# Optimization experiments

Hardware: AMD Instinct MI355X
Metric: run time of the kernel (lower is better)

## Reference

```python
import jax, jax.numpy as jnp
import numpy as np


def setup_inputs() -> dict:
    key = jax.random.key(0)
    ks = jax.random.split(key, 8)
    B, N, D = 8, 2048, 128
    s = 1.0 / float(np.sqrt(D))
    node = jax.random.normal(ks[0], (B, N, D), dtype=jnp.float32)
    node_mask = jax.random.randint(ks[1], (B, N), 0, 2, dtype=jnp.int32)
    punctuation_graph = jax.random.randint(ks[2], (B, N, N), 0, 2, dtype=jnp.int32)
    w_nw = jax.random.uniform(ks[3], (1, D), jnp.float32, -s, s)
    b_nw = jax.random.uniform(ks[4], (1,), jnp.float32, -s, s)
    w_self = jax.random.uniform(ks[5], (D, D), jnp.float32, -s, s)
    b_self = jax.random.uniform(ks[6], (D,), jnp.float32, -s, s)
    w_punct = jax.random.uniform(ks[7], (D, D), jnp.float32, -s, s)
    return {"node": node, "node_mask": node_mask, "punctuation_graph": punctuation_graph,
            "w_nw": w_nw, "b_nw": b_nw, "w_self": w_self, "b_self": b_self,
            "w_punct": w_punct, "iteration_steps": 2}


def reference(node, node_mask, punctuation_graph, w_nw, b_nw, w_self, b_self, w_punct, iteration_steps):
    B, N, D = node.shape
    # dd_graph = mask outer product with zeroed diagonal; graph = dd_graph * punctuation_graph
    eye = jnp.eye(N, dtype=punctuation_graph.dtype)
    dd = node_mask[:, None, :] * node_mask[:, :, None] * (1 - eye)[None, :, :]  # [B,N,N]
    graph = dd * punctuation_graph  # [B,N,N] int, binary
    nbr_num = graph.sum(-1)  # [B,N]
    # replace_masked_values(nbr_num, nbr_num>=1, 1): nodes with no neighbors get denom 1
    nbr_f = jnp.where(nbr_num >= 1, nbr_num.astype(node.dtype), jnp.asarray(1.0, node.dtype))
    gmask = graph > 0
    weights = []
    x = node
    for _ in range(iteration_steps):  # small fixed step count
        dw = jax.nn.sigmoid(jnp.einsum('bnd,od->bno', x, w_nw) + b_nw)[..., 0]  # [B,N]
        weights.append(dw)
        self_info = jnp.einsum('bnd,ed->bne', x, w_self) + b_self  # [B,N,D]
        info_p = jnp.einsum('bnd,ed->bne', x, w_punct)  # [B,N,D]
        # node_weight[b,i,j] = dw[b,j] where graph[b,i,j] else 0
        nw = jnp.where(gmask, dw[:, None, :], jnp.asarray(0.0, x.dtype))  # [B,N,N]
        agg = jnp.einsum('bnm,bmd->bnd', nw, info_p) / nbr_f[..., None]
        x = jax.nn.relu(self_info + agg)
    all_weight = jnp.stack(weights, axis=1)  # [B, steps, N]
    return x, all_weight
```

## Files before the change

kernel.cpp:

```cpp
#include <hip/hip_runtime.h>
#include <hip/hip_bf16.h>

#define BB 8
#define NN 2048
#define DD 128

typedef __attribute__((ext_vector_type(8))) __bf16 bf16x8;
typedef __attribute__((ext_vector_type(4))) float f32x4;
typedef __attribute__((ext_vector_type(4))) int   i32x4;

static __device__ __forceinline__ unsigned short f2bf(float f) {
    union { float f; unsigned u; } v; v.f = f;
    unsigned r = (v.u + 0x7FFFu + ((v.u >> 16) & 1u)) >> 16;
    return (unsigned short)r;
}
static __device__ __forceinline__ float bf2f(unsigned short b) {
    union { unsigned u; float f; } v; v.u = ((unsigned)b) << 16;
    return v.f;
}

__global__ __launch_bounds__(256) void kernB0(
    const float* __restrict__ x,
    const float* __restrict__ w_nw, const float* __restrict__ b_nw,
    const float* __restrict__ w_self, const float* __restrict__ b_self,
    const float* __restrict__ w_punct,
    float* __restrict__ si_out,
    unsigned short* __restrict__ yne_out,
    unsigned short* __restrict__ yT_out,
    float* __restrict__ aw_out)
{
    __shared__ unsigned short xt[64*32];
    __shared__ unsigned short wst[128*32];
    __shared__ unsigned short wpt[128*32];
    __shared__ float wnw_l[DD];
    __shared__ float red[256];
    __shared__ float dw_l[64];
    __shared__ unsigned short ytl[128*72];

    const int n0 = blockIdx.x * 64;
    const int t  = threadIdx.x;
    const int b  = n0 >> 11;
    const int nb = n0 & (NN - 1);

    if (t < DD) wnw_l[t] = w_nw[t];
    __syncthreads();

    const int wave = t >> 6, lane = t & 63;
    const int wm = wave >> 1, wn = wave & 1;
    const int quad = lane >> 4, l16 = lane & 15;

    const int n_loc = t >> 2, dq = t & 3;
    const int we = t >> 1,   wh = t & 1;

    f32x4 accs[2][4] = {}; f32x4 accp[2][4] = {};
    float dwpart = 0.f;

    #pragma unroll
    for (int kk = 0; kk < 4; ++kk) {
        const int k0 = kk * 32;
        {
            const float* xs = x + (size_t)(n0 + n_loc) * DD + k0 + dq * 8;
            f32x4 a = *(const f32x4*)xs;
            f32x4 c = *(const f32x4*)(xs + 4);
            const float* wv = &wnw_l[k0 + dq * 8];
            dwpart += a.x*wv[0] + a.y*wv[1] + a.z*wv[2] + a.w*wv[3]
                    + c.x*wv[4] + c.y*wv[5] + c.z*wv[6] + c.w*wv[7];
            unsigned q0 = f2bf(a.x) | ((unsigned)f2bf(a.y) << 16);
            unsigned q1 = f2bf(a.z) | ((unsigned)f2bf(a.w) << 16);
            unsigned q2 = f2bf(c.x) | ((unsigned)f2bf(c.y) << 16);
            unsigned q3 = f2bf(c.z) | ((unsigned)f2bf(c.w) << 16);
            i32x4 pw = {(int)q0,(int)q1,(int)q2,(int)q3};
            *(i32x4*)&xt[n_loc*32 + dq*8] = pw;
        }
        {
            const float* s1 = w_self  + (size_t)we * DD + k0 + wh*16;
            const float* s2 = w_punct + (size_t)we * DD + k0 + wh*16;
            f32x4 a0 = *(const f32x4*)s1;      f32x4 a1 = *(const f32x4*)(s1+4);
            f32x4 a2 = *(const f32x4*)(s1+8);  f32x4 a3 = *(const f32x4*)(s1+12);
            unsigned q0 = f2bf(a0.x) | ((unsigned)f2bf(a0.y)<<16);
            unsigned q1 = f2bf(a0.z) | ((unsigned)f2bf(a0.w)<<16);
            unsigned q2 = f2bf(a1.x) | ((unsigned)f2bf(a1.y)<<16);
            unsigned q3 = f2bf(a1.z) | ((unsigned)f2bf(a1.w)<<16);
            unsigned q4 = f2bf(a2.x) | ((unsigned)f2bf(a2.y)<<16);
            unsigned q5 = f2bf(a2.z) | ((unsigned)f2bf(a2.w)<<16);
            unsigned q6 = f2bf(a3.x) | ((unsigned)f2bf(a3.y)<<16);
            unsigned q7 = f2bf(a3.z) | ((unsigned)f2bf(a3.w)<<16);
            i32x4 pw0 = {(int)q0,(int)q1,(int)q2,(int)q3};
            i32x4 pw1 = {(int)q4,(int)q5,(int)q6,(int)q7};
            *(i32x4*)&wst[we*32 + wh*16]     = pw0;
            *(i32x4*)&wst[we*32 + wh*16 + 8] = pw1;
            f32x4 c0 = *(const f32x4*)s2;      f32x4 c1 = *(const f32x4*)(s2+4);
            f32x4 c2 = *(const f32x4*)(s2+8);  f32x4 c3 = *(const f32x4*)(s2+12);
            unsigned r0 = f2bf(c0.x) | ((unsigned)f2bf(c0.y)<<16);
            unsigned r1 = f2bf(c0.z) | ((unsigned)f2bf(c0.w)<<16);
            unsigned r2 = f2bf(c1.x) | ((unsigned)f2bf(c1.y)<<16);
            unsigned r3 = f2bf(c1.z) | ((unsigned)f2bf(c1.w)<<16);
            unsigned r4 = f2bf(c2.x) | ((unsigned)f2bf(c2.y)<<16);
            unsigned r5 = f2bf(c2.z) | ((unsigned)f2bf(c2.w)<<16);
            unsigned r6 = f2bf(c3.x) | ((unsigned)f2bf(c3.y)<<16);
            unsigned r7 = f2bf(c3.z) | ((unsigned)f2bf(c3.w)<<16);
            i32x4 pv0 = {(int)r0,(int)r1,(int)r2,(int)r3};
            i32x4 pv1 = {(int)r4,(int)r5,(int)r6,(int)r7};
            *(i32x4*)&wpt[we*32 + wh*16]     = pv0;
            *(i32x4*)&wpt[we*32 + wh*16 + 8] = pv1;
        }
        __syncthreads();
        bf16x8 af[2], bs[4], bp[4];
        #pragma unroll
        for (int mt = 0; mt < 2; ++mt)
            af[mt] = *(const bf16x8*)&xt[(wm*32 + mt*16 + l16)*32 + quad*8];
        #pragma unroll
        for (int nt = 0; nt < 4; ++nt) {
            const int er = wn*64 + nt*16 + l16;
            bs[nt] = *(const bf16x8*)&wst[er*32 + quad*8];
            bp[nt] = *(const bf16x8*)&wpt[er*32 + quad*8];
        }
        #pragma unroll
        for (int mt = 0; mt < 2; ++mt)
            #pragma unroll
            for (int nt = 0; nt < 4; ++nt) {
                accs[mt][nt] = __builtin_amdgcn_mfma_f32_16x16x32_bf16(af[mt], bs[nt], accs[mt][nt], 0, 0, 0);
                accp[mt][nt] = __builtin_amdgcn_mfma_f32_16x16x32_bf16(af[mt], bp[nt], accp[mt][nt], 0, 0, 0);
            }
        __syncthreads();
    }

    red[t] = dwpart;
    __syncthreads();
    if (t < 64) {
        float s = red[4*t] + red[4*t+1] + red[4*t+2] + red[4*t+3] + b_nw[0];
        float dv = 1.f / (1.f + __expf(-s));
        dw_l[t] = dv;
        aw_out[(size_t)b * 2 * NN + nb + t] = dv;
    }
    __syncthreads();

    #pragma unroll
    for (int mt = 0; mt < 2; ++mt) {
        #pragma unroll
        for (int nt = 0; nt < 4; ++nt) {
            const int e = wn*64 + nt*16 + l16;
            const float bsv = b_self[e];
            #pragma unroll
            for (int r = 0; r < 4; ++r) {
                const int nl = wm*32 + mt*16 + quad*4 + r;
                const size_t idx = (size_t)(n0 + nl) * DD + e;
                si_out[idx] = accs[mt][nt][r] + bsv;
                const float yv = dw_l[nl] * accp[mt][nt][r];
                const unsigned short ub = f2bf(yv);
                yne_out[idx] = ub;
                ytl[e*72 + nl] = ub;
            }
        }
    }
    __syncthreads();
    {
        const int e = t >> 1, half = t & 1;
        const i32x4* src = (const i32x4*)&ytl[e*72 + half*32];
        i32x4 v0 = src[0], v1 = src[1], v2 = src[2], v3 = src[3];
        i32x4* dst = (i32x4*)(yT_out + (size_t)(b*DD + e) * NN + nb + half*32);
        dst[0] = v0; dst[1] = v1; dst[2] = v2; dst[3] = v3;
    }
}

__global__ __launch_bounds__(256) void kernP3(
    const int* __restrict__ punct, const int* __restrict__ mask,
    const float* __restrict__ w_self, const float* __restrict__ w_punct,
    unsigned* __restrict__ pk, float* __restrict__ scale_g, float* __restrict__ pdm_g,
    unsigned short* __restrict__ wsb, unsigned short* __restrict__ wpb)
{
    const int bid = blockIdx.x;
    const int t = threadIdx.x;

    if (bid >= 2048) {
        const int cb = bid - 2048;
        const float* src = (cb < 8) ? w_self : w_punct;
        unsigned short* dst = (cb < 8) ? wsb : wpb;
        const size_t i0 = (size_t)(cb & 7) * 2048 + (size_t)t * 8;
        f32x4 a = *(const f32x4*)(src + i0);
        f32x4 c = *(const f32x4*)(src + i0 + 4);
        unsigned q0 = f2bf(a.x) | ((unsigned)f2bf(a.y) << 16);
        unsigned q1 = f2bf(a.z) | ((unsigned)f2bf(a.w) << 16);
        unsigned q2 = f2bf(c.x) | ((unsigned)f2bf(c.y) << 16);
        unsigned q3 = f2bf(c.z) | ((unsigned)f2bf(c.w) << 16);
        i32x4 pw = {(int)q0, (int)q1, (int)q2, (int)q3};
        *(i32x4*)(dst + i0) = pw;
        return;
    }

    const int wave = t >> 6, lane = t & 63;
    const int row0 = bid * 8 + wave * 2;
    const int b = row0 >> 11;
    const int* mrow = mask + (size_t)b * NN;

    unsigned mw = 0;
    #pragma unroll
    for (int q = 0; q < 8; ++q) {
        i32x4 m = *(const i32x4*)(mrow + lane * 32 + q * 4);
        unsigned nib = (m.x & 1) | ((m.y & 1) << 1) | ((m.z & 1) << 2) | ((m.w & 1) << 3);
        mw |= nib << (4 * q);
    }

    #pragma unroll
    for (int r = 0; r < 2; ++r) {
        const int row = row0 + r;
        const int i = row & (NN - 1);
        const int mi = mrow[i];
        if (mi == 0) {
            if (lane == 0) { scale_g[row] = 0.f; pdm_g[row] = 0.f; }
            continue;
        }
        const int* prow = punct + (size_t)row * NN;
        i32x4 v[8];
        #pragma unroll
        for (int q = 0; q < 8; ++q)
            v[q] = *(const i32x4*)(prow + lane * 32 + q * 4);
        unsigned wd = 0;
        #pragma unroll
        for (int q = 0; q < 8; ++q) {
            unsigned nib = (v[q].x & 1) | ((v[q].y & 1) << 1)
                         | ((v[q].z & 1) << 2) | ((v[q].w & 1) << 3);
            wd |= nib << (4 * q);
        }
        wd &= mw;
        pk[(size_t)row * 64 + lane] = wd;

        int acc = __popc(wd);
        if ((i >> 5) == lane) acc += (int)((wd >> (i & 31)) & 1u) << 16;
        #pragma unroll
        for (int o = 32; o > 0; o >>= 1) acc += __shfl_xor(acc, o, 64);
        if (lane == 0) {
            const int nall = acc & 0xFFFF;
            const int pd   = acc >> 16;
            const int nbr  = nall - pd;
            scale_g[row] = 1.f / (float)(nbr < 1 ? 1 : nbr);
            pdm_g[row]   = (float)pd;
        }
    }
}

#define OFF_SCL   0u
#define OFF_PDM   256u
#define OFF_WNW   512u
#define OFF_DW    1024u
#define OFF_A     1280u
#define OFF_XT4   1280u
#define OFF_RED   (1280u + 16384u)
#define OFF_B     25856u
#define OFF_WST   25856u
#define OFF_WPT   (25856u + 8192u)
#define OFF_YTL   (25856u + 16384u)
#define SMEM_CB   60672u

__global__ __launch_bounds__(256) void kernCB(
    const unsigned* __restrict__ pk,
    const float* __restrict__ scale_g, const float* __restrict__ pdm_g,
    const unsigned short* __restrict__ yT0,
    const unsigned short* __restrict__ yne0,
    float* si,
    const unsigned short* __restrict__ wsb, const unsigned short* __restrict__ wpb,
    const float* __restrict__ w_nw, const float* __restrict__ b_nw,
    const float* __restrict__ b_self,
    unsigned short* __restrict__ yT1,
    float* __restrict__ aw1)
{
    __shared__ char smem[SMEM_CB];
    float*          scl_l = (float*)(smem + OFF_SCL);
    float*          pdm_l = (float*)(smem + OFF_PDM);
    float*          wnw_l = (float*)(smem + OFF_WNW);
    float*          dw_l  = (float*)(smem + OFF_DW);
    unsigned*       pPk   = (unsigned*)(smem + OFF_A);
    unsigned short* xt4   = (unsigned short*)(smem + OFF_XT4);
    float*          red   = (float*)(smem + OFF_RED);
    f32x4*          accL  = (f32x4*)(smem + OFF_B);
    unsigned short* wst   = (unsigned short*)(smem + OFF_WST);
    unsigned short* wpt   = (unsigned short*)(smem + OFF_WPT);
    unsigned short* ytl   = (unsigned short*)(smem + OFF_YTL);

    const int t  = threadIdx.x;
    const int b  = blockIdx.x & 7;
    const int i0 = (blockIdx.x >> 3) * 64;
    const size_t rg0 = (size_t)b * NN + i0;

    #pragma unroll
    for (int r = 0; r < 4; ++r) {
        const int u   = r * 256 + t;
        const int row = u >> 4;
        const int wq  = (u & 15) * 4;
        i32x4 v = *(const i32x4*)(pk + (rg0 + row) * 64 + wq);
        *(i32x4*)&pPk[row * 68 + wq] = v;
    }
    if (t < 64)                   scl_l[t]      = scale_g[rg0 + t];
    else if (t < 128)             pdm_l[t-64]   = pdm_g[rg0 + t - 64];
    else                          wnw_l[t-128]  = w_nw[t-128];
    __syncthreads();

    const int wave = t >> 6, lane = t & 63;
    const int kh = wave >> 1, eh = wave & 1;
    const int quad = lane >> 4, l16 = lane & 15;
    const unsigned short* yTb = yT0 + (size_t)b * DD * NN;

    f32x4 acc[4][4] = {};
    #pragma unroll 4
    for (int ks = 0; ks < 32; ++ks) {
        const int kk = kh * 32 + ks;
        bf16x8 bfr[4];
        #pragma unroll
        for (int nt = 0; nt < 4; ++nt) {
            const int e = eh*64 + nt*16 + l16;
            bfr[nt] = *(const bf16x8*)(yTb + (size_t)e * NN + kk*32 + quad*8);
        }
        bf16x8 af[4];
        #pragma unroll
        for (int mt = 0; mt < 4; ++mt) {
            const unsigned w = pPk[(mt*16 + l16) * 68 + kk];
            const unsigned by = (w >> (quad * 8)) & 0xFFu;
            i32x4 ex;
            ex.x = (int)((((by &   1u) << 7) + ((by &   2u) << 22)) * 0x7Fu);
            ex.y = (int)((((by &   4u) << 5) + ((by &   8u) << 20)) * 0x7Fu);
            ex.z = (int)((((by &  16u) << 3) + ((by &  32u) << 18)) * 0x7Fu);
            ex.w = (int)((((by &  64u) << 1) + ((by & 128u) << 16)) * 0x7Fu);
            union { i32x4 i; bf16x8 h; } cv; cv.i = ex;
            af[mt] = cv.h;
        }
        #pragma unroll
        for (int mt = 0; mt < 4; ++mt)
            #pragma unroll
            for (int nt = 0; nt < 4; ++nt)
                acc[mt][nt] = __builtin_amdgcn_mfma_f32_16x16x32_bf16(af[mt], bfr[nt], acc[mt][nt], 0, 0, 0);
    }

    __syncthreads();
    if (kh == 1) {
        #pragma unroll
        for (int mt = 0; mt < 4; ++mt)
            #pragma unroll
            for (int nt = 0; nt < 4; ++nt)
                accL[(eh*16 + mt*4 + nt)*64 + lane] = acc[mt][nt];
    }
    __syncthreads();

    if (kh == 0) {
        #pragma unroll
        for (int mt = 0; mt < 4; ++mt) {
            float part[4] = {0.f, 0.f, 0.f, 0.f};
            #pragma unroll
            for (int nt = 0; nt < 4; ++nt) {
                f32x4 o = accL[(eh*16 + mt*4 + nt)*64 + lane];
                const int e = eh*64 + nt*16 + l16;
                const float wv = wnw_l[e];
                #pragma unroll
                for (int r = 0; r < 4; ++r) {
                    const int row = mt*16 + quad*4 + r;
                    const size_t idx = (rg0 + row) * DD + e;
                    const float yv = bf2f(yne0[idx]);
                    float xv = si[idx]
                             + scl_l[row] * (acc[mt][nt][r] + o[r] - pdm_l[row] * yv);
                    xv = fmaxf(xv, 0.f);
                    xt4[((e >> 5) * 64 + row) * 32 + (e & 31)] = f2bf(xv);
                    part[r] += xv * wv;
                }
            }
            #pragma unroll
            for (int r = 0; r < 4; ++r) {
                const int row = mt*16 + quad*4 + r;
                red[row * 32 + eh*16 + l16] = part[r];
            }
        }
    }
    __syncthreads();

    if (t < 64) {
        float s = b_nw[0];
        #pragma unroll 8
        for (int c = 0; c < 32; ++c) s += red[t * 32 + c];
        float dv = 1.f / (1.f + __expf(-s));
        dw_l[t] = dv;
        aw1[(size_t)b * 2 * NN + i0 + t] = dv;
    }
    __syncthreads();

    const int wm = kh, wn = eh;
    const int we = t >> 1, wh = t & 1;

    f32x4 accs[2][4] = {}; f32x4 accp[2][4] = {};

    #pragma unroll
    for (int kk = 0; kk < 4; ++kk) {
        const int k0 = kk * 32;
        {
            const unsigned short* s1 = wsb + (size_t)we * DD + k0 + wh*16;
            const unsigned short* s2 = wpb + (size_t)we * DD + k0 + wh*16;
            i32x4 a0 = *(const i32x4*)s1;
            i32x4 a1 = *(const i32x4*)(s1 + 8);
            *(i32x4*)&wst[we*32 + wh*16]     = a0;
            *(i32x4*)&wst[we*32 + wh*16 + 8] = a1;
            i32x4 c0 = *(const i32x4*)s2;
            i32x4 c1 = *(const i32x4*)(s2 + 8);
            *(i32x4*)&wpt[we*32 + wh*16]     = c0;
            *(i32x4*)&wpt[we*32 + wh*16 + 8] = c1;
        }
        __syncthreads();
        bf16x8 af[2], bs[4], bp[4];
        #pragma unroll
        for (int mt = 0; mt < 2; ++mt)
            af[mt] = *(const bf16x8*)&xt4[(kk*64 + wm*32 + mt*16 + l16)*32 + quad*8];
        #pragma unroll
        for (int nt = 0; nt < 4; ++nt) {
            const int er = wn*64 + nt*16 + l16;
            bs[nt] = *(const bf16x8*)&wst[er*32 + quad*8];
            bp[nt] = *(const bf16x8*)&wpt[er*32 + quad*8];
        }
        #pragma unroll
        for (int mt = 0; mt < 2; ++mt)
            #pragma unroll
            for (int nt = 0; nt < 4; ++nt) {
                accs[mt][nt] = __builtin_amdgcn_mfma_f32_16x16x32_bf16(af[mt], bs[nt], accs[mt][nt], 0, 0, 0);
                accp[mt][nt] = __builtin_amdgcn_mfma_f32_16x16x32_bf16(af[mt], bp[nt], accp[mt][nt], 0, 0, 0);
            }
        __syncthreads();
    }

    #pragma unroll
    for (int mt = 0; mt < 2; ++mt) {
        #pragma unroll
        for (int nt = 0; nt < 4; ++nt) {
            const int e = wn*64 + nt*16 + l16;
            const float bsv = b_self[e];
            #pragma unroll
            for (int r = 0; r < 4; ++r) {
                const int nl = wm*32 + mt*16 + quad*4 + r;
                const size_t idx = (rg0 + nl) * DD + e;
                const float yv = dw_l[nl] * accp[mt][nt][r];
                const unsigned short ub = f2bf(yv);
                const float yvr = bf2f(ub);
                si[idx] = accs[mt][nt][r] + bsv - scl_l[nl] * pdm_l[nl] * yvr;
                ytl[e*72 + nl] = ub;
            }
        }
    }
    __syncthreads();
    {
        const int e = t >> 1, half = t & 1;
        const i32x4* src = (const i32x4*)&ytl[e*72 + half*32];
        i32x4 v0 = src[0], v1 = src[1], v2 = src[2], v3 = src[3];
        i32x4* dst = (i32x4*)(yT1 + (size_t)(b*DD + e) * NN + i0 + half*32);
        dst[0] = v0; dst[1] = v1; dst[2] = v2; dst[3] = v3;
    }
}

__global__ __launch_bounds__(256) void kernC4(
    const unsigned* __restrict__ pk,
    const float* __restrict__ scale_g,
    const unsigned short* __restrict__ yT,
    const float* __restrict__ sip,
    float* __restrict__ x_out)
{
    __shared__ unsigned pPk[64 * 68];
    __shared__ float scale_l[64];
    __shared__ f32x4 accL[2][16][64];

    const int t  = threadIdx.x;
    const int b  = blockIdx.x & 7;
    const int i0 = (blockIdx.x >> 3) * 64;
    const size_t rg0 = (size_t)b * NN + i0;

    #pragma unroll
    for (int r = 0; r < 4; ++r) {
        const int u   = r * 256 + t;
        const int row = u >> 4;
        const int wq  = (u & 15) * 4;
        i32x4 v = *(const i32x4*)(pk + (rg0 + row) * 64 + wq);
        *(i32x4*)&pPk[row * 68 + wq] = v;
    }
    if (t < 64) scale_l[t] = scale_g[rg0 + t];
    __syncthreads();

    const int wave = t >> 6, lane = t & 63;
    const int kh = wave >> 1, eh = wave & 1;
    const int quad = lane >> 4, l16 = lane & 15;
    const unsigned short* yTb = yT + (size_t)b * DD * NN;

    f32x4 acc[4][4] = {};

    #pragma unroll 4
    for (int ks = 0; ks < 32; ++ks) {
        const int kk = kh * 32 + ks;
        bf16x8 bfr[4];
        #pragma unroll
        for (int nt = 0; nt < 4; ++nt) {
            const int e = eh*64 + nt*16 + l16;
            bfr[nt] = *(const bf16x8*)(yTb + (size_t)e * NN + kk*32 + quad*8);
        }
        bf16x8 af[4];
        #pragma unroll
        for (int mt = 0; mt < 4; ++mt) {
            const unsigned w = pPk[(mt*16 + l16) * 68 + kk];
            const unsigned by = (w >> (quad * 8)) & 0xFFu;
            i32x4 ex;
            ex.x = (int)((((by &   1u) << 7) + ((by &   2u) << 22)) * 0x7Fu);
            ex.y = (int)((((by &   4u) << 5) + ((by &   8u) << 20)) * 0x7Fu);
            ex.z = (int)((((by &  16u) << 3) + ((by &  32u) << 18)) * 0x7Fu);
            ex.w = (int)((((by &  64u) << 1) + ((by & 128u) << 16)) * 0x7Fu);
            union { i32x4 i; bf16x8 h; } cv; cv.i = ex;
            af[mt] = cv.h;
        }
        #pragma unroll
        for (int mt = 0; mt < 4; ++mt)
            #pragma unroll
            for (int nt = 0; nt < 4; ++nt)
                acc[mt][nt] = __builtin_amdgcn_mfma_f32_16x16x32_bf16(af[mt], bfr[nt], acc[mt][nt], 0, 0, 0);
    }

    __syncthreads();
    if (kh == 1) {
        #pragma unroll
        for (int mt = 0; mt < 4; ++mt)
            #pragma unroll
            for (int nt = 0; nt < 4; ++nt)
                accL[eh][mt*4 + nt][lane] = acc[mt][nt];
    }
    __syncthreads();
    if (kh == 0) {
        #pragma unroll
        for (int mt = 0; mt < 4; ++mt) {
            #pragma unroll
            for (int nt = 0; nt < 4; ++nt) {
                f32x4 o = accL[eh][mt*4 + nt][lane];
                const int e = eh*64 + nt*16 + l16;
                #pragma unroll
                for (int r = 0; r < 4; ++r) {
                    const int row = mt*16 + quad*4 + r;
                    const size_t idx = (rg0 + row) * DD + e;
                    float v = sip[idx] + scale_l[row] * (acc[mt][nt][r] + o[r]);
                    x_out[idx] = fmaxf(v, 0.f);
                }
            }
        }
    }
}

extern "C" void kernel_launch(void* const* d_in, const int* in_sizes, int n_in,
                              void* d_out, int out_size, void* d_ws, size_t ws_size,
                              hipStream_t stream) {
    const float* node   = (const float*)d_in[0];
    const int*   mask   = (const int*)  d_in[1];
    const int*   punct  = (const int*)  d_in[2];
    const float* w_nw   = (const float*)d_in[3];
    const float* b_nw   = (const float*)d_in[4];
    const float* w_self = (const float*)d_in[5];
    const float* b_self = (const float*)d_in[6];
    const float* w_punct= (const float*)d_in[7];

    float* xout = (float*)d_out;
    float* aw   = xout + (size_t)BB * NN * DD;

    char* w = (char*)d_ws;
    float*          si   = (float*)w;
    unsigned short* yne0 = (unsigned short*)(w + (8u  << 20));
    unsigned short* yT0  = (unsigned short*)(w + (12u << 20));
    unsigned*       pk   = (unsigned*)(w + (16u << 20));
    float*          scl  = (float*)(w + (20u << 20));
    float*          pdm  = (float*)(w + (20u << 20) + (64u << 10));
    unsigned short* wsb  = (unsigned short*)(w + (21u << 20));
    unsigned short* wpb  = (unsigned short*)(w + (21u << 20) + (32u << 10));
    unsigned short* yT1  = (unsigned short*)(w + (24u << 20));

    kernB0<<<dim3(256),  dim3(256), 0, stream>>>(node, w_nw, b_nw, w_self,
                                                 b_self, w_punct,
                                                 si, yne0, yT0, aw);
    kernP3<<<dim3(2064), dim3(256), 0, stream>>>(punct, mask, w_self, w_punct,
                                                 pk, scl, pdm, wsb, wpb);
    kernCB<<<dim3(256),  dim3(256), 0, stream>>>(pk, scl, pdm, yT0, yne0, si,
                                                 wsb, wpb, w_nw, b_nw, b_self,
                                                 yT1, aw + NN);
    kernC4<<<dim3(256),  dim3(256), 0, stream>>>(pk, scl, yT1, si, xout);
}
```

Before: 263.8 us.

## Fuse graph bit-packing and weight bf16 conversion into aggregation kernel

Removes the separate packing kernel and packs the punctuation graph rows and mask directly inside the first aggregation kernel, writing packed bits to shared memory and to global for the later kernel. Weight matrices are converted from fp32 to bf16 on the fly in each block instead of being precomputed. This saves a launch and a global round trip of packed data. In exchange, the large int32 graph read is spread over only 256 blocks with serial per-wave row loops, which may reduce memory-level parallelism, and the weight conversion is repeated redundantly per block.

```diff
diff --git a/kernel.cpp b/kernel.cpp
--- a/kernel.cpp
+++ b/kernel.cpp
@@ -163,82 +163,6 @@
     }
 }
 
-__global__ __launch_bounds__(256) void kernP3(
-    const int* __restrict__ punct, const int* __restrict__ mask,
-    const float* __restrict__ w_self, const float* __restrict__ w_punct,
-    unsigned* __restrict__ pk, float* __restrict__ scale_g, float* __restrict__ pdm_g,
-    unsigned short* __restrict__ wsb, unsigned short* __restrict__ wpb)
-{
-    const int bid = blockIdx.x;
-    const int t = threadIdx.x;
-
-    if (bid >= 2048) {
-        const int cb = bid - 2048;
-        const float* src = (cb < 8) ? w_self : w_punct;
-        unsigned short* dst = (cb < 8) ? wsb : wpb;
-        const size_t i0 = (size_t)(cb & 7) * 2048 + (size_t)t * 8;
-        f32x4 a = *(const f32x4*)(src + i0);
-        f32x4 c = *(const f32x4*)(src + i0 + 4);
-        unsigned q0 = f2bf(a.x) | ((unsigned)f2bf(a.y) << 16);
-        unsigned q1 = f2bf(a.z) | ((unsigned)f2bf(a.w) << 16);
-        unsigned q2 = f2bf(c.x) | ((unsigned)f2bf(c.y) << 16);
-        unsigned q3 = f2bf(c.z) | ((unsigned)f2bf(c.w) << 16);
-        i32x4 pw = {(int)q0, (int)q1, (int)q2, (int)q3};
-        *(i32x4*)(dst + i0) = pw;
-        return;
-    }
-
-    const int wave = t >> 6, lane = t & 63;
-    const int row0 = bid * 8 + wave * 2;
-    const int b = row0 >> 11;
-    const int* mrow = mask + (size_t)b * NN;
-
-    unsigned mw = 0;
-    #pragma unroll
-    for (int q = 0; q < 8; ++q) {
-        i32x4 m = *(const i32x4*)(mrow + lane * 32 + q * 4);
-        unsigned nib = (m.x & 1) | ((m.y & 1) << 1) | ((m.z & 1) << 2) | ((m.w & 1) << 3);
-        mw |= nib << (4 * q);
-    }
-
-    #pragma unroll
-    for (int r = 0; r < 2; ++r) {
-        const int row = row0 + r;
-        const int i = row & (NN - 1);
-        const int mi = mrow[i];
-        if (mi == 0) {
-            if (lane == 0) { scale_g[row] = 0.f; pdm_g[row] = 0.f; }
-            continue;
-        }
-        const int* prow = punct + (size_t)row * NN;
-        i32x4 v[8];
-        #pragma unroll
-        for (int q = 0; q < 8; ++q)
-            v[q] = *(const i32x4*)(prow + lane * 32 + q * 4);
-        unsigned wd = 0;
-        #pragma unroll
-        for (int q = 0; q < 8; ++q) {
-            unsigned nib = (v[q].x & 1) | ((v[q].y & 1) << 1)
-                         | ((v[q].z & 1) << 2) | ((v[q].w & 1) << 3);
-            wd |= nib << (4 * q);
-        }
-        wd &= mw;
-        pk[(size_t)row * 64 + lane] = wd;
-
-        int acc = __popc(wd);
-        if ((i >> 5) == lane) acc += (int)((wd >> (i & 31)) & 1u) << 16;
-        #pragma unroll
-        for (int o = 32; o > 0; o >>= 1) acc += __shfl_xor(acc, o, 64);
-        if (lane == 0) {
-            const int nall = acc & 0xFFFF;
-            const int pd   = acc >> 16;
-            const int nbr  = nall - pd;
-            scale_g[row] = 1.f / (float)(nbr < 1 ? 1 : nbr);
-            pdm_g[row]   = (float)pd;
-        }
-    }
-}
-
 #define OFF_SCL   0u
 #define OFF_PDM   256u
 #define OFF_WNW   512u
@@ -252,15 +176,16 @@
 #define OFF_YTL   (25856u + 16384u)
 #define SMEM_CB   60672u
 
-__global__ __launch_bounds__(256) void kernCB(
-    const unsigned* __restrict__ pk,
-    const float* __restrict__ scale_g, const float* __restrict__ pdm_g,
+__global__ __launch_bounds__(256) void kernCBP(
+    const int* __restrict__ punct, const int* __restrict__ mask,
     const unsigned short* __restrict__ yT0,
     const unsigned short* __restrict__ yne0,
     float* si,
-    const unsigned short* __restrict__ wsb, const unsigned short* __restrict__ wpb,
+    const float* __restrict__ w_self, const float* __restrict__ w_punct,
     const float* __restrict__ w_nw, const float* __restrict__ b_nw,
     const float* __restrict__ b_self,
+    unsigned* __restrict__ pk_g, float* __restrict__ scale_g,
+    float* __restrict__ pdm_g,
     unsigned short* __restrict__ yT1,
     float* __restrict__ aw1)
 {
@@ -282,20 +207,61 @@
     const int i0 = (blockIdx.x >> 3) * 64;
     const size_t rg0 = (size_t)b * NN + i0;
 
-    #pragma unroll
-    for (int r = 0; r < 4; ++r) {
-        const int u   = r * 256 + t;
-        const int row = u >> 4;
-        const int wq  = (u & 15) * 4;
-        i32x4 v = *(const i32x4*)(pk + (rg0 + row) * 64 + wq);
-        *(i32x4*)&pPk[row * 68 + wq] = v;
-    }
-    if (t < 64)                   scl_l[t]      = scale_g[rg0 + t];
-    else if (t < 128)             pdm_l[t-64]   = pdm_g[rg0 + t - 64];
-    else                          wnw_l[t-128]  = w_nw[t-128];
-    __syncthreads();
-
     const int wave = t >> 6, lane = t & 63;
+
+    {
+        const int* mrow = mask + (size_t)b * NN;
+        unsigned mw = 0;
+        #pragma unroll
+        for (int q = 0; q < 8; ++q) {
+            i32x4 m = *(const i32x4*)(mrow + lane * 32 + q * 4);
+            unsigned nib = (m.x & 1) | ((m.y & 1) << 1) | ((m.z & 1) << 2) | ((m.w & 1) << 3);
+            mw |= nib << (4 * q);
+        }
+        for (int rr = 0; rr < 16; ++rr) {
+            const int rl = wave * 16 + rr;
+            const int gi = i0 + rl;
+            const int mi = mrow[gi];
+            if (mi == 0) {
+                if (lane == 0) {
+                    scl_l[rl] = 0.f; pdm_l[rl] = 0.f;
+                    scale_g[rg0 + rl] = 0.f; pdm_g[rg0 + rl] = 0.f;
+                }
+                continue;
+            }
+            const int* prow = punct + (rg0 + rl) * NN;
+            i32x4 v[8];
+            #pragma unroll
+            for (int q = 0; q < 8; ++q)
+                v[q] = *(const i32x4*)(prow + lane * 32 + q * 4);
+            unsigned wd = 0;
+            #pragma unroll
+            for (int q = 0; q < 8; ++q) {
+                unsigned nib = (v[q].x & 1) | ((v[q].y & 1) << 1)
+                             | ((v[q].z & 1) << 2) | ((v[q].w & 1) << 3);
+                wd |= nib << (4 * q);
+            }
+            wd &= mw;
+            pPk[rl * 68 + lane] = wd;
+            pk_g[(rg0 + rl) * 64 + lane] = wd;
+
+            int acc = __popc(wd);
+            if ((gi >> 5) == lane) acc += (int)((wd >> (gi & 31)) & 1u) << 16;
+            #pragma unroll
+            for (int o = 32; o > 0; o >>= 1) acc += __shfl_xor(acc, o, 64);
+            if (lane == 0) {
+                const int nall = acc & 0xFFFF;
+                const int pd   = acc >> 16;
+                const int nbr  = nall - pd;
+                const float sc = 1.f / (float)(nbr < 1 ? 1 : nbr);
+                scl_l[rl] = sc; pdm_l[rl] = (float)pd;
+                scale_g[rg0 + rl] = sc; pdm_g[rg0 + rl] = (float)pd;
+            }
+        }
+    }
+    if (t < 128) wnw_l[t] = w_nw[t];
+    __syncthreads();
+
     const int kh = wave >> 1, eh = wave & 1;
     const int quad = lane >> 4, l16 = lane & 15;
     const unsigned short* yTb = yT0 + (size_t)b * DD * NN;
@@ -389,16 +355,36 @@
     for (int kk = 0; kk < 4; ++kk) {
         const int k0 = kk * 32;
         {
-            const unsigned short* s1 = wsb + (size_t)we * DD + k0 + wh*16;
-            const unsigned short* s2 = wpb + (size_t)we * DD + k0 + wh*16;
-            i32x4 a0 = *(const i32x4*)s1;
-            i32x4 a1 = *(const i32x4*)(s1 + 8);
-            *(i32x4*)&wst[we*32 + wh*16]     = a0;
-            *(i32x4*)&wst[we*32 + wh*16 + 8] = a1;
-            i32x4 c0 = *(const i32x4*)s2;
-            i32x4 c1 = *(const i32x4*)(s2 + 8);
-            *(i32x4*)&wpt[we*32 + wh*16]     = c0;
-            *(i32x4*)&wpt[we*32 + wh*16 + 8] = c1;
+            const float* s1 = w_self  + (size_t)we * DD + k0 + wh*16;
+            const float* s2 = w_punct + (size_t)we * DD + k0 + wh*16;
+            f32x4 a0 = *(const f32x4*)s1;      f32x4 a1 = *(const f32x4*)(s1+4);
+            f32x4 a2 = *(const f32x4*)(s1+8);  f32x4 a3 = *(const f32x4*)(s1+12);
+            unsigned q0 = f2bf(a0.x) | ((unsigned)f2bf(a0.y)<<16);
+            unsigned q1 = f2bf(a0.z) | ((unsigned)f2bf(a0.w)<<16);
+            unsigned q2 = f2bf(a1.x) | ((unsigned)f2bf(a1.y)<<16);
+            unsigned q3 = f2bf(a1.z) | ((unsigned)f2bf(a1.w)<<16);
+            unsigned q4 = f2bf(a2.x) | ((unsigned)f2bf(a2.y)<<16);
+            unsigned q5 = f2bf(a2.z) | ((unsigned)f2bf(a2.w)<<16);
+            unsigned q6 = f2bf(a3.x) | ((unsigned)f2bf(a3.y)<<16);
+            unsigned q7 = f2bf(a3.z) | ((unsigned)f2bf(a3.w)<<16);
+            i32x4 pw0 = {(int)q0,(int)q1,(int)q2,(int)q3};
+            i32x4 pw1 = {(int)q4,(int)q5,(int)q6,(int)q7};
+            *(i32x4*)&wst[we*32 + wh*16]     = pw0;
+            *(i32x4*)&wst[we*32 + wh*16 + 8] = pw1;
+            f32x4 c0 = *(const f32x4*)s2;      f32x4 c1 = *(const f32x4*)(s2+4);
+            f32x4 c2 = *(const f32x4*)(s2+8);  f32x4 c3 = *(const f32x4*)(s2+12);
+            unsigned r0 = f2bf(c0.x) | ((unsigned)f2bf(c0.y)<<16);
+            unsigned r1 = f2bf(c0.z) | ((unsigned)f2bf(c0.w)<<16);
+            unsigned r2 = f2bf(c1.x) | ((unsigned)f2bf(c1.y)<<16);
+            unsigned r3 = f2bf(c1.z) | ((unsigned)f2bf(c1.w)<<16);
+            unsigned r4 = f2bf(c2.x) | ((unsigned)f2bf(c2.y)<<16);
+            unsigned r5 = f2bf(c2.z) | ((unsigned)f2bf(c2.w)<<16);
+            unsigned r6 = f2bf(c3.x) | ((unsigned)f2bf(c3.y)<<16);
+            unsigned r7 = f2bf(c3.z) | ((unsigned)f2bf(c3.w)<<16);
+            i32x4 pv0 = {(int)r0,(int)r1,(int)r2,(int)r3};
+            i32x4 pv1 = {(int)r4,(int)r5,(int)r6,(int)r7};
+            *(i32x4*)&wpt[we*32 + wh*16]     = pv0;
+            *(i32x4*)&wpt[we*32 + wh*16 + 8] = pv1;
         }
         __syncthreads();
         bf16x8 af[2], bs[4], bp[4];
@@ -562,17 +548,14 @@
     unsigned*       pk   = (unsigned*)(w + (16u << 20));
     float*          scl  = (float*)(w + (20u << 20));
     float*          pdm  = (float*)(w + (20u << 20) + (64u << 10));
-    unsigned short* wsb  = (unsigned short*)(w + (21u << 20));
-    unsigned short* wpb  = (unsigned short*)(w + (21u << 20) + (32u << 10));
     unsigned short* yT1  = (unsigned short*)(w + (24u << 20));
 
-    kernB0<<<dim3(256),  dim3(256), 0, stream>>>(node, w_nw, b_nw, w_self,
+    kernB0 <<<dim3(256), dim3(256), 0, stream>>>(node, w_nw, b_nw, w_self,
                                                  b_self, w_punct,
                                                  si, yne0, yT0, aw);
-    kernP3<<<dim3(2064), dim3(256), 0, stream>>>(punct, mask, w_self, w_punct,
-                                                 pk, scl, pdm, wsb, wpb);
-    kernCB<<<dim3(256),  dim3(256), 0, stream>>>(pk, scl, pdm, yT0, yne0, si,
-                                                 wsb, wpb, w_nw, b_nw, b_self,
+    kernCBP<<<dim3(256), dim3(256), 0, stream>>>(punct, mask, yT0, yne0, si,
+                                                 w_self, w_punct, w_nw, b_nw,
+                                                 b_self, pk, scl, pdm,
                                                  yT1, aw + NN);
-    kernC4<<<dim3(256),  dim3(256), 0, stream>>>(pk, scl, yT1, si, xout);
+    kernC4 <<<dim3(256), dim3(256), 0, stream>>>(pk, scl, yT1, si, xout);
 }
```

After: 264.2 us. No clear change (+0.1%).
